# Kernel tuning notes

Hardware: AMD Instinct MI355X
Metric: run time of the kernel (lower is better)

The kernel has to match this reference:

```python
import jax, jax.numpy as jnp
import numpy as np

B, T, IN, H, OUT, L = 1024, 128, 32, 256, 32, 3  # batch, times, input_dim, hidden_dim, output_dim, num_layers
STEP = 0.05  # odeint rk4 step_size; times grid is aligned to it


def lipswish(x):
    return 0.909 * x * jax.nn.sigmoid(x)


def setup_inputs() -> dict:
    key = jax.random.key(0)
    ks = jax.random.split(key, 4)
    coeffs = jax.random.normal(ks[0], (B, T, IN), dtype=jnp.float32)
    times = jnp.arange(T, dtype=jnp.float32) * STEP
    # learned parameters
    W_init = jax.random.normal(ks[1], (IN, H), dtype=jnp.float32) * (1.0 / np.sqrt(IN))
    b_init = jnp.zeros((H,), dtype=jnp.float32)
    # vector field f: L lipswish hidden layers + final linear, all H->H
    Wf = jax.random.normal(ks[2], (L + 1, H, H), dtype=jnp.float32) * (1.0 / np.sqrt(H))
    bf = jnp.zeros((L + 1, H), dtype=jnp.float32)
    Wd = jax.random.normal(ks[3], (H, OUT), dtype=jnp.float32) * (1.0 / np.sqrt(H))
    bd = jnp.zeros((OUT,), dtype=jnp.float32)
    return dict(coeffs=coeffs, times=times, W_init=W_init, b_init=b_init,
                Wf=Wf, bf=bf, Wd=Wd, bd=bd)


def reference(coeffs, times, W_init, b_init, Wf, bf, Wd, bd):
    # vector field func.f(t, y): autonomous MLP (inject_noise=False, so g unused)
    def f(y):
        h = y
        for i in range(L):
            h = lipswish(h @ Wf[i] + bf[i])
        return h @ Wf[L] + bf[L]

    # y0 = initial(X.evaluate(times))[:, 0, :] -> only the first time point seeds the state
    y0 = coeffs[:, 0, :] @ W_init + b_init  # [B, H]

    dts = times[1:] - times[:-1]  # each interval = one RK4 step (grid aligned to step_size)

    def step(y, dt):
        k1 = f(y)
        k2 = f(y + 0.5 * dt * k1)
        k3 = f(y + 0.5 * dt * k2)
        k4 = f(y + dt * k3)
        y_next = y + (dt / 6.0) * (k1 + 2.0 * k2 + 2.0 * k3 + k4)
        return y_next, y_next

    _, ys = jax.lax.scan(step, y0, dts)  # [T-1, B, H]
    z = jnp.concatenate([y0[None], ys], axis=0)  # [T, B, H]
    z = jnp.transpose(z, (1, 0, 2))  # [B, T, H]
    return z @ Wd + bd  # [B, T, OUT]
```

## Files before the change

### kernel.cpp

```cpp
#include <hip/hip_runtime.h>


#define T_ 128
#define IN_ 32
#define H_ 256

typedef _Float16 half8 __attribute__((ext_vector_type(8)));
typedef _Float16 half4 __attribute__((ext_vector_type(4)));
typedef float f32x4 __attribute__((ext_vector_type(4)));

__device__ __forceinline__ f32x4 mfma16(half8 a, half8 b, f32x4 c) {
    return __builtin_amdgcn_mfma_f32_16x16x32_f16(a, b, c, 0, 0, 0);
}

__device__ __forceinline__ half4 cvt4(f32x4 v) {
    half4 h;
    h[0] = (_Float16)v[0]; h[1] = (_Float16)v[1];
    h[2] = (_Float16)v[2]; h[3] = (_Float16)v[3];
    return h;
}

__device__ __forceinline__ f32x4 lips4(f32x4 v) {
    f32x4 r;
#pragma unroll
    for (int e = 0; e < 4; ++e) {
        float x = v[e];
        r[e] = 0.909f * x * __builtin_amdgcn_rcpf(1.f + __expf(-x));
    }
    return r;
}

#define RDH(KS, BUF) (*(const half8*)(ht + (BUF) + (((KS) & 1) ? (po + ((KS)-1)*64) : (pe + (KS)*64))))
#define RDA(C, KS)   (*(const half8*)(w0b + (C)*8192 + (KS)*1024))

#define LOADB(BUF) do { b0=RDH(0,BUF); b1=RDH(1,BUF); b2=RDH(2,BUF); b3=RDH(3,BUF); \
                        b4=RDH(4,BUF); b5=RDH(5,BUF); b6=RDH(6,BUF); b7=RDH(7,BUF); } while (0)

#define L0_KS(KS, BK) do { \
    half8 a0_=RDA(0,KS), a1_=RDA(1,KS), a2_=RDA(2,KS), a3_=RDA(3,KS); \
    acc0=mfma16(a0_,BK,acc0); acc1=mfma16(a1_,BK,acc1); \
    acc2=mfma16(a2_,BK,acc2); acc3=mfma16(a3_,BK,acc3); } while (0)
#define LAYER_L0 do { L0_KS(0,b0); L0_KS(1,b1); L0_KS(2,b2); L0_KS(3,b3); \
                      L0_KS(4,b4); L0_KS(5,b5); L0_KS(6,b6); L0_KS(7,b7); } while (0)

#define REG_KS(KS, BK) do { \
    acc0=mfma16(wreg[0][KS],BK,acc0); acc1=mfma16(wreg[1][KS],BK,acc1); \
    acc2=mfma16(wreg[2][KS],BK,acc2); acc3=mfma16(wreg[3][KS],BK,acc3); } while (0)
#define LAYER_REG do { REG_KS(0,b0); REG_KS(1,b1); REG_KS(2,b2); REG_KS(3,b3); \
                       REG_KS(4,b4); REG_KS(5,b5); REG_KS(6,b6); REG_KS(7,b7); } while (0)

#define LD4(D0,D1,D2,D3,P,F) do { \
    D0=*(const half8*)((P)+((F)+0)*1024); D1=*(const half8*)((P)+((F)+1)*1024); \
    D2=*(const half8*)((P)+((F)+2)*1024); D3=*(const half8*)((P)+((F)+3)*1024); } while (0)

#define MA4(ACC) do { ACC=mfma16(sa0,b0,ACC); ACC=mfma16(sa1,b1,ACC); \
                      ACC=mfma16(sa2,b2,ACC); ACC=mfma16(sa3,b3,ACC); } while (0)
#define MB4(ACC) do { ACC=mfma16(sb0,b4,ACC); ACC=mfma16(sb1,b5,ACC); \
                      ACC=mfma16(sb2,b6,ACC); ACC=mfma16(sb3,b7,ACC); } while (0)

#define STREAM_LAYER(WP, PN) do { \
    LD4(sb0,sb1,sb2,sb3, WP, 4);   MA4(acc0); \
    LD4(sa0,sa1,sa2,sa3, WP, 8);   MB4(acc0); \
    LD4(sb0,sb1,sb2,sb3, WP, 12);  MA4(acc1); \
    LD4(sa0,sa1,sa2,sa3, WP, 16);  MB4(acc1); \
    LD4(sb0,sb1,sb2,sb3, WP, 20);  MA4(acc2); \
    LD4(sa0,sa1,sa2,sa3, WP, 24);  MB4(acc2); \
    LD4(sb0,sb1,sb2,sb3, WP, 28);  MA4(acc3); \
    LD4(sa0,sa1,sa2,sa3, PN, 0);   MB4(acc3); } while (0)

#define ACC_INIT(LY) do { \
    acc0 = *(const f32x4*)(bias4 + (LY)*H_ +  0); \
    acc1 = *(const f32x4*)(bias4 + (LY)*H_ + 16); \
    acc2 = *(const f32x4*)(bias4 + (LY)*H_ + 32); \
    acc3 = *(const f32x4*)(bias4 + (LY)*H_ + 48); } while (0)

#define ACT_STORE(BUF) do { \
    *(half4*)(ht + (BUF) + wo0)        = cvt4(lips4(acc0)); \
    *(half4*)(ht + (BUF) + (wo0^32))   = cvt4(lips4(acc1)); \
    *(half4*)(ht + (BUF) + (wo0^64))   = cvt4(lips4(acc2)); \
    *(half4*)(ht + (BUF) + (wo0^96))   = cvt4(lips4(acc3)); } while (0)

#define STORE_Y(BUF, V0, V1, V2, V3) do { \
    *(half4*)(ht + (BUF) + wo0)        = cvt4(V0); \
    *(half4*)(ht + (BUF) + (wo0^32))   = cvt4(V1); \
    *(half4*)(ht + (BUF) + (wo0^64))   = cvt4(V2); \
    *(half4*)(ht + (BUF) + (wo0^96))   = cvt4(V3); } while (0)

__global__ __launch_bounds__(256)
void pack_kernel(const float* __restrict__ Wf, _Float16* __restrict__ wpack)
{
    int idx = blockIdx.x * 256 + threadIdx.x;
    int lane = idx & 63, ks = (idx >> 6) & 7, c = (idx >> 9) & 3;
    int w = (idx >> 11) & 3, ly = (idx >> 13) & 1;
    int col = w*64 + c*16 + (lane & 15);
    int row = ks*32 + (lane >> 4) * 8;
    const float* src = Wf + ((size_t)(ly + 2) * H_ + row) * H_ + col;
    half8 v;
#pragma unroll
    for (int j = 0; j < 8; ++j) v[j] = (_Float16)src[(size_t)j * H_];
    *(half8*)(wpack + (size_t)idx * 8) = v;
}

__global__ __attribute__((amdgpu_flat_work_group_size(256, 256), amdgpu_waves_per_eu(1, 1)))
void ncde_kernel(const float* __restrict__ coeffs,
                 const float* __restrict__ times,
                 const float* __restrict__ W_init,
                 const float* __restrict__ b_init,
                 const float* __restrict__ Wf,
                 const float* __restrict__ bfv,
                 const _Float16* __restrict__ wpack,
                 _Float16* __restrict__ ybuf)
{
    extern __shared__ char smem[];
    _Float16* w0   = (_Float16*)smem;
    char*     ht   = smem + 131072;
    float*    bias = (float*)(smem + 131072 + 16384);
    float*    tlds = (float*)(smem + 131072 + 16384 + 4096);

    const int tid = threadIdx.x;
    const int l   = tid & 63;
    const int w   = tid >> 6;
    const int lr  = l & 15;
    const int lk  = l >> 4;
    const int bc  = blockIdx.x;

    const int swz  = (lr & 7) << 4;
    const int base = lr*512 + ((lk*16) ^ (swz & 0x30));
    const int sswz = swz & 0x40;
    const int pe   = base + sswz;
    const int po   = base + 64 - sswz;
    const int wo0  = lr*512 + (((w*128) | (lk*8)) ^ swz);
    const char*  w0b   = (const char*)w0 + (size_t)w * 32768 + l * 16;
    const float* bias4 = bias + w*64 + lk*4;
    const char*  wpb2  = (const char*)wpack + (size_t)(0*4 + w) * 32768 + l * 16;
    const char*  wpb3  = (const char*)wpack + (size_t)(1*4 + w) * 32768 + l * 16;

    for (int i = tid; i < 4 * H_; i += 256) bias[i] = bfv[i];
    if (tid < T_) tlds[tid] = times[tid];

    for (int e = tid; e < 8192; e += 256) {
        int ct = e >> 9, ks = (e >> 6) & 7, ln = e & 63;
        const float* src = Wf + (size_t)(ks*32 + ((ln >> 4) << 3)) * H_ + ct*16 + (ln & 15);
        half8 v;
#pragma unroll
        for (int j = 0; j < 8; ++j) v[j] = (_Float16)src[(size_t)j * H_];
        *(half8*)(w0 + (size_t)e * 8) = v;
    }

    half8 wreg[4][8];
#pragma unroll
    for (int c = 0; c < 4; ++c)
#pragma unroll
        for (int ks = 0; ks < 8; ++ks) {
            const float* src = Wf + ((size_t)H_ + ks*32 + lk*8) * H_ + w*64 + c*16 + lr;
            half8 v;
#pragma unroll
            for (int j = 0; j < 8; ++j) v[j] = (_Float16)src[(size_t)j * H_];
            wreg[c][ks] = v;
        }

    f32x4 y0v, y1v, y2v, y3v;
    {
        const float* crow = coeffs + (size_t)(bc*16 + lr) * (T_ * IN_);
#pragma unroll
        for (int c = 0; c < 4; ++c) {
            f32x4 acc;
#pragma unroll
            for (int r = 0; r < 4; ++r) {
                int col = w*64 + c*16 + lk*4 + r;
                float s = b_init[col];
                for (int k = 0; k < IN_; ++k)
                    s += crow[k] * W_init[(size_t)k * H_ + col];
                acc[r] = s;
            }
            if (c == 0) y0v = acc; else if (c == 1) y1v = acc;
            else if (c == 2) y2v = acc; else y3v = acc;
        }
    }

    STORE_Y(0, y0v, y1v, y2v, y3v);
    __syncthreads();
    {
        int drow = tid >> 4, dcb = (tid & 15) * 32, dsw = (drow & 7) << 4;
        const char* sp = ht + drow * 512;
        uint4 a = *(const uint4*)(sp + (dcb ^ dsw));
        uint4 bq = *(const uint4*)(sp + ((dcb + 16) ^ dsw));
        char* dst = (char*)ybuf + (size_t)(bc * T_) * 8192 + tid * 32;
        *(uint4*)dst = a; *(uint4*)(dst + 16) = bq;
    }

    half8 b0, b1, b2, b3, b4, b5, b6, b7;
    half8 sa0, sa1, sa2, sa3, sb0, sb1, sb2, sb3;
    LD4(sa0, sa1, sa2, sa3, wpb2, 0);

#pragma unroll 1
    for (int st = 0; st < T_ - 1; ++st) {
        float dt = tlds[st + 1] - tlds[st];
        f32x4 ks0v, ks1v, ks2v, ks3v;
#pragma unroll 1
        for (int s = 0; s < 4; ++s) {
            f32x4 acc0, acc1, acc2, acc3;
            ACC_INIT(0); LOADB(0);    LAYER_L0;             ACT_STORE(8192); __syncthreads();
            ACC_INIT(1); LOADB(8192); LAYER_REG;            ACT_STORE(0);    __syncthreads();
            ACC_INIT(2); LOADB(0);    STREAM_LAYER(wpb2, wpb3); ACT_STORE(8192); __syncthreads();
            ACC_INIT(3); LOADB(8192); STREAM_LAYER(wpb3, wpb2);
            if (s == 0)      { ks0v = acc0;       ks1v = acc1;       ks2v = acc2;       ks3v = acc3; }
            else if (s < 3)  { ks0v += 2.f*acc0;  ks1v += 2.f*acc1;  ks2v += 2.f*acc2;  ks3v += 2.f*acc3; }
            else             { ks0v += acc0;      ks1v += acc1;      ks2v += acc2;      ks3v += acc3; }
            if (s < 3) {
                float cy = (s == 2) ? dt : 0.5f * dt;
                STORE_Y(0, y0v + cy*acc0, y1v + cy*acc1, y2v + cy*acc2, y3v + cy*acc3);
            } else {
                float c6 = dt * (1.f / 6.f);
                y0v += c6*ks0v; y1v += c6*ks1v; y2v += c6*ks2v; y3v += c6*ks3v;
                STORE_Y(0, y0v, y1v, y2v, y3v);
            }
            __syncthreads();
        }
        {
            int drow = tid >> 4, dcb = (tid & 15) * 32, dsw = (drow & 7) << 4;
            const char* sp = ht + drow * 512;
            uint4 a = *(const uint4*)(sp + (dcb ^ dsw));
            uint4 bq = *(const uint4*)(sp + ((dcb + 16) ^ dsw));
            char* dst = (char*)ybuf + (size_t)(bc * T_ + st + 1) * 8192 + tid * 32;
            *(uint4*)dst = a; *(uint4*)(dst + 16) = bq;
        }
    }
}

__global__ __launch_bounds__(64)
void proj_kernel(const _Float16* __restrict__ ybuf,
                 const float* __restrict__ Wd,
                 const float* __restrict__ bd,
                 float* __restrict__ out)
{
    const int l  = threadIdx.x;
    const int lr = l & 15, lk = l >> 4;
    const int bc = blockIdx.x;
    const int tg = blockIdx.y;

    half8 wd[2][8];
#pragma unroll
    for (int c = 0; c < 2; ++c)
#pragma unroll
        for (int ks = 0; ks < 8; ++ks) {
            const float* src = Wd + (size_t)(ks*32 + lk*8) * 32 + c*16 + lr;
            half8 v;
#pragma unroll
            for (int j = 0; j < 8; ++j) v[j] = (_Float16)src[(size_t)j * 32];
            wd[c][ks] = v;
        }
    f32x4 bd0 = *(const f32x4*)(bd + lk*4);
    f32x4 bd1 = *(const f32x4*)(bd + 16 + lk*4);

    for (int t = tg*16; t < tg*16 + 16; ++t) {
        const _Float16* yt = ybuf + ((size_t)(bc*T_) + t) * 4096;
        f32x4 a0 = f32x4{0.f,0.f,0.f,0.f}, a1 = f32x4{0.f,0.f,0.f,0.f};
#pragma unroll
        for (int ks = 0; ks < 8; ++ks) {
            half8 b = *(const half8*)(yt + lr*256 + ks*32 + lk*8);
            a0 = mfma16(wd[0][ks], b, a0);
            a1 = mfma16(wd[1][ks], b, a1);
        }
        float* op = out + ((size_t)(bc*16 + lr) * T_ + t) * 32;
        *(f32x4*)(op + lk*4)      = a0 + bd0;
        *(f32x4*)(op + 16 + lk*4) = a1 + bd1;
    }
}

extern "C" void kernel_launch(void* const* d_in, const int* in_sizes, int n_in,
                              void* d_out, int out_size, void* d_ws, size_t ws_size,
                              hipStream_t stream) {
    const float* coeffs = (const float*)d_in[0];
    const float* times  = (const float*)d_in[1];
    const float* W_init = (const float*)d_in[2];
    const float* b_init = (const float*)d_in[3];
    const float* Wf     = (const float*)d_in[4];
    const float* bfv    = (const float*)d_in[5];
    const float* Wd     = (const float*)d_in[6];
    const float* bd     = (const float*)d_in[7];
    _Float16* wpack = (_Float16*)d_ws;
    _Float16* ybuf  = (_Float16*)((char*)d_ws + 524288);
    float* out = (float*)d_out;

    hipLaunchKernelGGL(pack_kernel, dim3(64), dim3(256), 0, stream, Wf, wpack);

    const size_t lds_bytes = 131072 + 16384 + 4096 + 512;
    hipLaunchKernelGGL(ncde_kernel, dim3(64), dim3(256), lds_bytes, stream,
                       coeffs, times, W_init, b_init, Wf, bfv, wpack, ybuf);
    hipLaunchKernelGGL(proj_kernel, dim3(64, 8), dim3(64), 0, stream,
                       ybuf, Wd, bd, out);
}
```

Measured before the change: 2.070 ms.

## Stream layers 1-3 weights from global via six-group register ring buffer

Layer 1 no longer keeps its weights resident in 128 registers. It is now streamed from a packed global buffer like layers 2 and 3, which the pack kernel now builds for all three layers. A six-deep rotating set of register groups prefetches weights across layer boundaries and across steps. The barrier is replaced with an explicit lgkmcnt wait plus s_barrier and a sched_barrier, and the waves_per_eu constraint is dropped. This frees registers but adds global/L2 traffic on the latency-critical serial path, so it trades register pressure against memory latency.

```diff
diff --git a/kernel.cpp b/kernel.cpp
--- a/kernel.cpp
+++ b/kernel.cpp
@@ -29,6 +29,12 @@
     }
     return r;
 }
+
+#define SYNC() do {                                         \
+    asm volatile("s_waitcnt lgkmcnt(0)" ::: "memory");      \
+    __builtin_amdgcn_s_barrier();                           \
+    __builtin_amdgcn_sched_barrier(0);                      \
+} while (0)
 
 #define RDH(KS, BUF) (*(const half8*)(ht + (BUF) + (((KS) & 1) ? (po + ((KS)-1)*64) : (pe + (KS)*64))))
 #define RDA(C, KS)   (*(const half8*)(w0b + (C)*8192 + (KS)*1024))
@@ -43,30 +49,48 @@
 #define LAYER_L0 do { L0_KS(0,b0); L0_KS(1,b1); L0_KS(2,b2); L0_KS(3,b3); \
                       L0_KS(4,b4); L0_KS(5,b5); L0_KS(6,b6); L0_KS(7,b7); } while (0)
 
-#define REG_KS(KS, BK) do { \
-    acc0=mfma16(wreg[0][KS],BK,acc0); acc1=mfma16(wreg[1][KS],BK,acc1); \
-    acc2=mfma16(wreg[2][KS],BK,acc2); acc3=mfma16(wreg[3][KS],BK,acc3); } while (0)
-#define LAYER_REG do { REG_KS(0,b0); REG_KS(1,b1); REG_KS(2,b2); REG_KS(3,b3); \
-                       REG_KS(4,b4); REG_KS(5,b5); REG_KS(6,b6); REG_KS(7,b7); } while (0)
-
-#define LD4(D0,D1,D2,D3,P,F) do { \
-    D0=*(const half8*)((P)+((F)+0)*1024); D1=*(const half8*)((P)+((F)+1)*1024); \
-    D2=*(const half8*)((P)+((F)+2)*1024); D3=*(const half8*)((P)+((F)+3)*1024); } while (0)
-
-#define MA4(ACC) do { ACC=mfma16(sa0,b0,ACC); ACC=mfma16(sa1,b1,ACC); \
-                      ACC=mfma16(sa2,b2,ACC); ACC=mfma16(sa3,b3,ACC); } while (0)
-#define MB4(ACC) do { ACC=mfma16(sb0,b4,ACC); ACC=mfma16(sb1,b5,ACC); \
-                      ACC=mfma16(sb2,b6,ACC); ACC=mfma16(sb3,b7,ACC); } while (0)
-
-#define STREAM_LAYER(WP, PN) do { \
-    LD4(sb0,sb1,sb2,sb3, WP, 4);   MA4(acc0); \
-    LD4(sa0,sa1,sa2,sa3, WP, 8);   MB4(acc0); \
-    LD4(sb0,sb1,sb2,sb3, WP, 12);  MA4(acc1); \
-    LD4(sa0,sa1,sa2,sa3, WP, 16);  MB4(acc1); \
-    LD4(sb0,sb1,sb2,sb3, WP, 20);  MA4(acc2); \
-    LD4(sa0,sa1,sa2,sa3, WP, 24);  MB4(acc2); \
-    LD4(sb0,sb1,sb2,sb3, WP, 28);  MA4(acc3); \
-    LD4(sa0,sa1,sa2,sa3, PN, 0);   MB4(acc3); } while (0)
+#define LDB(A,B,C,D,G) do { \
+    A = *(const half8*)(wpb + (G)*4096);        \
+    B = *(const half8*)(wpb + (G)*4096 + 1024); \
+    C = *(const half8*)(wpb + (G)*4096 + 2048); \
+    D = *(const half8*)(wpb + (G)*4096 + 3072); } while (0)
+
+#define MAB(A,B,C,D, ACC, B0,B1,B2,B3) do { \
+    ACC = mfma16(A, B0, ACC); ACC = mfma16(B, B1, ACC); \
+    ACC = mfma16(C, B2, ACC); ACC = mfma16(D, B3, ACC); } while (0)
+
+#define STREAM_L1 do { \
+    MAB(s0a,s0b,s0c,s0d, acc0, b0,b1,b2,b3); LDB(s0a,s0b,s0c,s0d, 6); \
+    MAB(s1a,s1b,s1c,s1d, acc0, b4,b5,b6,b7); LDB(s1a,s1b,s1c,s1d, 7); \
+    MAB(s2a,s2b,s2c,s2d, acc1, b0,b1,b2,b3); LDB(s2a,s2b,s2c,s2d, 8); \
+    MAB(s3a,s3b,s3c,s3d, acc1, b4,b5,b6,b7); LDB(s3a,s3b,s3c,s3d, 9); \
+    MAB(s4a,s4b,s4c,s4d, acc2, b0,b1,b2,b3); LDB(s4a,s4b,s4c,s4d,10); \
+    MAB(s5a,s5b,s5c,s5d, acc2, b4,b5,b6,b7); LDB(s5a,s5b,s5c,s5d,11); \
+    MAB(s0a,s0b,s0c,s0d, acc3, b0,b1,b2,b3); LDB(s0a,s0b,s0c,s0d,12); \
+    MAB(s1a,s1b,s1c,s1d, acc3, b4,b5,b6,b7); LDB(s1a,s1b,s1c,s1d,13); \
+} while (0)
+
+#define STREAM_L2 do { \
+    MAB(s2a,s2b,s2c,s2d, acc0, b0,b1,b2,b3); LDB(s2a,s2b,s2c,s2d,14); \
+    MAB(s3a,s3b,s3c,s3d, acc0, b4,b5,b6,b7); LDB(s3a,s3b,s3c,s3d,15); \
+    MAB(s4a,s4b,s4c,s4d, acc1, b0,b1,b2,b3); LDB(s4a,s4b,s4c,s4d,16); \
+    MAB(s5a,s5b,s5c,s5d, acc1, b4,b5,b6,b7); LDB(s5a,s5b,s5c,s5d,17); \
+    MAB(s0a,s0b,s0c,s0d, acc2, b0,b1,b2,b3); LDB(s0a,s0b,s0c,s0d,18); \
+    MAB(s1a,s1b,s1c,s1d, acc2, b4,b5,b6,b7); LDB(s1a,s1b,s1c,s1d,19); \
+    MAB(s2a,s2b,s2c,s2d, acc3, b0,b1,b2,b3); LDB(s2a,s2b,s2c,s2d,20); \
+    MAB(s3a,s3b,s3c,s3d, acc3, b4,b5,b6,b7); LDB(s3a,s3b,s3c,s3d,21); \
+} while (0)
+
+#define STREAM_L3 do { \
+    MAB(s4a,s4b,s4c,s4d, acc0, b0,b1,b2,b3); LDB(s4a,s4b,s4c,s4d,22); \
+    MAB(s5a,s5b,s5c,s5d, acc0, b4,b5,b6,b7); LDB(s5a,s5b,s5c,s5d,23); \
+    MAB(s0a,s0b,s0c,s0d, acc1, b0,b1,b2,b3); LDB(s0a,s0b,s0c,s0d, 0); \
+    MAB(s1a,s1b,s1c,s1d, acc1, b4,b5,b6,b7); LDB(s1a,s1b,s1c,s1d, 1); \
+    MAB(s2a,s2b,s2c,s2d, acc2, b0,b1,b2,b3); LDB(s2a,s2b,s2c,s2d, 2); \
+    MAB(s3a,s3b,s3c,s3d, acc2, b4,b5,b6,b7); LDB(s3a,s3b,s3c,s3d, 3); \
+    MAB(s4a,s4b,s4c,s4d, acc3, b0,b1,b2,b3); LDB(s4a,s4b,s4c,s4d, 4); \
+    MAB(s5a,s5b,s5c,s5d, acc3, b4,b5,b6,b7); LDB(s5a,s5b,s5c,s5d, 5); \
+} while (0)
 
 #define ACC_INIT(LY) do { \
     acc0 = *(const f32x4*)(bias4 + (LY)*H_ +  0); \
@@ -90,18 +114,22 @@
 void pack_kernel(const float* __restrict__ Wf, _Float16* __restrict__ wpack)
 {
     int idx = blockIdx.x * 256 + threadIdx.x;
-    int lane = idx & 63, ks = (idx >> 6) & 7, c = (idx >> 9) & 3;
-    int w = (idx >> 11) & 3, ly = (idx >> 13) & 1;
+    int lane = idx & 63;
+    int f5   = (idx >> 6) & 31;
+    int rest = idx >> 11;
+    int ly   = rest % 3;
+    int w    = rest / 3;
+    int c = f5 >> 3, ks = f5 & 7;
     int col = w*64 + c*16 + (lane & 15);
     int row = ks*32 + (lane >> 4) * 8;
-    const float* src = Wf + ((size_t)(ly + 2) * H_ + row) * H_ + col;
+    const float* src = Wf + ((size_t)(ly + 1) * H_ + row) * H_ + col;
     half8 v;
 #pragma unroll
     for (int j = 0; j < 8; ++j) v[j] = (_Float16)src[(size_t)j * H_];
     *(half8*)(wpack + (size_t)idx * 8) = v;
 }
 
-__global__ __attribute__((amdgpu_flat_work_group_size(256, 256), amdgpu_waves_per_eu(1, 1)))
+__global__ __attribute__((amdgpu_flat_work_group_size(256, 256)))
 void ncde_kernel(const float* __restrict__ coeffs,
                  const float* __restrict__ times,
                  const float* __restrict__ W_init,
@@ -132,11 +160,15 @@
     const int wo0  = lr*512 + (((w*128) | (lk*8)) ^ swz);
     const char*  w0b   = (const char*)w0 + (size_t)w * 32768 + l * 16;
     const float* bias4 = bias + w*64 + lk*4;
-    const char*  wpb2  = (const char*)wpack + (size_t)(0*4 + w) * 32768 + l * 16;
-    const char*  wpb3  = (const char*)wpack + (size_t)(1*4 + w) * 32768 + l * 16;
+    const char*  wpb   = (const char*)wpack + (size_t)w * 98304 + l * 16;
 
     for (int i = tid; i < 4 * H_; i += 256) bias[i] = bfv[i];
     if (tid < T_) tlds[tid] = times[tid];
+
+    half8 s0a,s0b,s0c,s0d, s1a,s1b,s1c,s1d, s2a,s2b,s2c,s2d,
+          s3a,s3b,s3c,s3d, s4a,s4b,s4c,s4d, s5a,s5b,s5c,s5d;
+    LDB(s0a,s0b,s0c,s0d, 0); LDB(s1a,s1b,s1c,s1d, 1); LDB(s2a,s2b,s2c,s2d, 2);
+    LDB(s3a,s3b,s3c,s3d, 3); LDB(s4a,s4b,s4c,s4d, 4); LDB(s5a,s5b,s5c,s5d, 5);
 
     for (int e = tid; e < 8192; e += 256) {
         int ct = e >> 9, ks = (e >> 6) & 7, ln = e & 63;
@@ -146,18 +178,6 @@
         for (int j = 0; j < 8; ++j) v[j] = (_Float16)src[(size_t)j * H_];
         *(half8*)(w0 + (size_t)e * 8) = v;
     }
-
-    half8 wreg[4][8];
-#pragma unroll
-    for (int c = 0; c < 4; ++c)
-#pragma unroll
-        for (int ks = 0; ks < 8; ++ks) {
-            const float* src = Wf + ((size_t)H_ + ks*32 + lk*8) * H_ + w*64 + c*16 + lr;
-            half8 v;
-#pragma unroll
-            for (int j = 0; j < 8; ++j) v[j] = (_Float16)src[(size_t)j * H_];
-            wreg[c][ks] = v;
-        }
 
     f32x4 y0v, y1v, y2v, y3v;
     {
@@ -190,8 +210,6 @@
     }
 
     half8 b0, b1, b2, b3, b4, b5, b6, b7;
-    half8 sa0, sa1, sa2, sa3, sb0, sb1, sb2, sb3;
-    LD4(sa0, sa1, sa2, sa3, wpb2, 0);
 
 #pragma unroll 1
     for (int st = 0; st < T_ - 1; ++st) {
@@ -200,10 +218,10 @@
 #pragma unroll 1
         for (int s = 0; s < 4; ++s) {
             f32x4 acc0, acc1, acc2, acc3;
-            ACC_INIT(0); LOADB(0);    LAYER_L0;             ACT_STORE(8192); __syncthreads();
-            ACC_INIT(1); LOADB(8192); LAYER_REG;            ACT_STORE(0);    __syncthreads();
-            ACC_INIT(2); LOADB(0);    STREAM_LAYER(wpb2, wpb3); ACT_STORE(8192); __syncthreads();
-            ACC_INIT(3); LOADB(8192); STREAM_LAYER(wpb3, wpb2);
+            ACC_INIT(0); LOADB(0);    LAYER_L0;  ACT_STORE(8192); SYNC();
+            ACC_INIT(1); LOADB(8192); STREAM_L1; ACT_STORE(0);    SYNC();
+            ACC_INIT(2); LOADB(0);    STREAM_L2; ACT_STORE(8192); SYNC();
+            ACC_INIT(3); LOADB(8192); STREAM_L3;
             if (s == 0)      { ks0v = acc0;       ks1v = acc1;       ks2v = acc2;       ks3v = acc3; }
             else if (s < 3)  { ks0v += 2.f*acc0;  ks1v += 2.f*acc1;  ks2v += 2.f*acc2;  ks3v += 2.f*acc3; }
             else             { ks0v += acc0;      ks1v += acc1;      ks2v += acc2;      ks3v += acc3; }
@@ -215,7 +233,7 @@
                 y0v += c6*ks0v; y1v += c6*ks1v; y2v += c6*ks2v; y3v += c6*ks3v;
                 STORE_Y(0, y0v, y1v, y2v, y3v);
             }
-            __syncthreads();
+            SYNC();
         }
         {
             int drow = tid >> 4, dcb = (tid & 15) * 32, dsw = (drow & 7) << 4;
@@ -283,7 +301,7 @@
     _Float16* ybuf  = (_Float16*)((char*)d_ws + 524288);
     float* out = (float*)d_out;
 
-    hipLaunchKernelGGL(pack_kernel, dim3(64), dim3(256), 0, stream, Wf, wpack);
+    hipLaunchKernelGGL(pack_kernel, dim3(96), dim3(256), 0, stream, Wf, wpack);
 
     const size_t lds_bytes = 131072 + 16384 + 4096 + 512;
     hipLaunchKernelGGL(ncde_kernel, dim3(64), dim3(256), lds_bytes, stream,
```

Measured after the change: 2.908 ms. 1.41x slower.
